# Performance work log

Measured on AMD Instinct MI355X. Metric: run time of the kernel, lower is better.

The kernel has to match this reference:

```python
import jax, jax.numpy as jnp
import numpy as np

N = 4096
IN_DIM = 512
NHEADS = 12
HEAD_DIM = 64


def setup_inputs() -> dict:
    key = jax.random.key(0)
    k_g, k_adj, k_wk, k_wq, k_hw = jax.random.split(key, 5)
    g = jax.random.normal(k_g, (N, IN_DIM), dtype=jnp.float32)
    # binary adjacency, broadcastable over the head axis of the [q,k,h] scores
    adj = jax.random.randint(k_adj, (N, N, 1), 0, 2).astype(jnp.float32)
    Wk = 0.002 * jax.random.normal(k_wk, (NHEADS, HEAD_DIM, IN_DIM), dtype=jnp.float32)
    Wq = 0.002 * jax.random.normal(k_wq, (NHEADS, HEAD_DIM, IN_DIM), dtype=jnp.float32)
    Hw = 0.002 * jax.random.normal(k_hw, (NHEADS, NHEADS), dtype=jnp.float32)
    Bk = jnp.zeros((NHEADS, HEAD_DIM), dtype=jnp.float32)
    Bq = jnp.zeros((NHEADS, HEAD_DIM), dtype=jnp.float32)
    betas = jnp.ones((NHEADS,), dtype=jnp.float32) / np.sqrt(HEAD_DIM).astype(np.float32)
    return {"g": g, "adj": adj, "Wk": Wk, "Wq": Wq, "Hw": Hw, "Bk": Bk, "Bq": Bq, "betas": betas}


def reference(g, adj, Wk, Wq, Hw, Bk, Bq, betas):
    def energy(g_):
        K = jnp.einsum('kd,hzd->khz', g_, Wk) + Bk          # [N, h, z]
        Q = jnp.einsum('qd,hzd->qhz', g_, Wq) + Bq          # [N, h, z]
        A1 = jnp.einsum('h,qhz,khz->hqk', betas, Q, K)      # [h, q, k]
        A11 = (jnp.transpose(A1, (1, 2, 0)) @ Hw) * adj      # [q, k, h], adjacency-gated
        A11 = jnp.where(A11 == 0, -jnp.inf, A11)
        A21 = jax.nn.logsumexp(A11, axis=1)                  # [q, h]
        A21 = jnp.where(A21 == -jnp.inf, 0.0, A21)
        A31 = A21.sum(0)                                     # [h]
        return ((-1.0 / betas) * A31).sum()
    # the module's __call__ returns (energy, dE/dg)
    return jax.value_and_grad(energy)(g)
```

## Files before the change

kernel.cpp:

```cpp
#include <hip/hip_runtime.h>
#include <stdint.h>

#define N_TOK 4096
#define DIM_IN 512
#define NH 12
#define HD 64
#define CDIM 768

using f32x4  = __attribute__((ext_vector_type(4))) float;
using f32x16 = __attribute__((ext_vector_type(16))) float;
using bf16x8 = __attribute__((ext_vector_type(8))) short;

static __device__ __forceinline__ unsigned short f2bf(float f){
    union { float f; unsigned int u; } v; v.f = f;
    unsigned int r = v.u + 0x7fffu + ((v.u >> 16) & 1u);
    return (unsigned short)(r >> 16);
}

__global__ __launch_bounds__(256) void proj_kernel(
    const float* __restrict__ g, const float* __restrict__ W,
    const float* __restrict__ B, const float* __restrict__ scale,
    unsigned short* __restrict__ out)
{
    __shared__ float at[16][68];
    __shared__ float bt[16][68];
    const int n0 = blockIdx.x * 64, c0 = blockIdx.y * 64;
    const int t  = threadIdx.x;
    const int tx = t & 15, ty = t >> 4;
    const int lr = t >> 2, lk = (t & 3) * 4;
    float acc[4][4] = {};
    for (int d0 = 0; d0 < DIM_IN; d0 += 16){
        __syncthreads();
        f32x4 gv = *(const f32x4*)&g[(size_t)(n0 + lr) * DIM_IN + d0 + lk];
        at[lk+0][lr] = gv[0]; at[lk+1][lr] = gv[1]; at[lk+2][lr] = gv[2]; at[lk+3][lr] = gv[3];
        f32x4 wv = *(const f32x4*)&W[(size_t)(c0 + lr) * DIM_IN + d0 + lk];
        bt[lk+0][lr] = wv[0]; bt[lk+1][lr] = wv[1]; bt[lk+2][lr] = wv[2]; bt[lk+3][lr] = wv[3];
        __syncthreads();
        #pragma unroll
        for (int kk = 0; kk < 16; kk++){
            f32x4 av = *(const f32x4*)&at[kk][ty*4];
            f32x4 bv = *(const f32x4*)&bt[kk][tx*4];
            #pragma unroll
            for (int i = 0; i < 4; i++)
                #pragma unroll
                for (int j = 0; j < 4; j++)
                    acc[i][j] += av[i] * bv[j];
        }
    }
    #pragma unroll
    for (int i = 0; i < 4; i++){
        const int n = n0 + ty*4 + i;
        #pragma unroll
        for (int j = 0; j < 4; j++){
            const int c = c0 + tx*4 + j;
            float v = acc[i][j] + B[c];
            if (scale) v *= scale[c >> 6];
            out[(size_t)n * CDIM + c] = f2bf(v);
        }
    }
}

#define TKF 32
#define KBS 776

__global__ __launch_bounds__(256, 2) void fwd_kernel(
    const unsigned short* __restrict__ Qb, const unsigned short* __restrict__ Kh,
    const float* __restrict__ adj, const float* __restrict__ HwG,
    float* __restrict__ l_ws, int seg_len)
{
    __shared__ unsigned short kbuf[TKF][KBS];
    __shared__ float hw[NH][12];
    const int t = threadIdx.x;
    if (t < NH * 12) hw[t / 12][t % 12] = HwG[t];
    const int lane = t & 63, wave = t >> 6;
    const int quad = lane >> 4, col = lane & 15;
    const int qt0 = blockIdx.x * 64 + wave * 16;
    const int kstart = blockIdx.y * seg_len;

    bf16x8 af[NH][2];
    {
        const int arow = qt0 + col;
        #pragma unroll
        for (int h = 0; h < NH; h++)
            #pragma unroll
            for (int kk = 0; kk < 2; kk++)
                af[h][kk] = *(const bf16x8*)&Qb[(size_t)arow * CDIM + h*HD + kk*32 + quad*8];
    }
    f32x4 l4[4][3];
    #pragma unroll
    for (int r = 0; r < 4; r++)
        #pragma unroll
        for (int j = 0; j < 3; j++)
            l4[r][j] = (f32x4){0.f,0.f,0.f,0.f};

    for (int kc = kstart; kc < kstart + seg_len; kc += TKF){
        __syncthreads();
        #pragma unroll
        for (int i = 0; i < 12; i++){
            const int idx = t + 256 * i;
            const int row = idx / 96, cc = (idx % 96) * 8;
            *(bf16x8*)&kbuf[row][cc] = *(const bf16x8*)&Kh[(size_t)(kc + row) * CDIM + cc];
        }
        __syncthreads();
        #pragma unroll
        for (int sub = 0; sub < 2; sub++){
            const int k0 = kc + sub * 16;
            f32x4 tv[4][3];
            #pragma unroll
            for (int r = 0; r < 4; r++)
                #pragma unroll
                for (int j = 0; j < 3; j++)
                    tv[r][j] = (f32x4){0.f,0.f,0.f,0.f};
            #pragma unroll
            for (int h = 0; h < NH; h++){
                bf16x8 b0 = *(const bf16x8*)&kbuf[sub*16 + col][h*HD + quad*8];
                bf16x8 b1 = *(const bf16x8*)&kbuf[sub*16 + col][h*HD + 32 + quad*8];
                f32x4 s = {0.f,0.f,0.f,0.f};
                s = __builtin_amdgcn_mfma_f32_16x16x32_bf16(af[h][0], b0, s, 0, 0, 0);
                s = __builtin_amdgcn_mfma_f32_16x16x32_bf16(af[h][1], b1, s, 0, 0, 0);
                f32x4 w0 = *(const f32x4*)&hw[h][0];
                f32x4 w1 = *(const f32x4*)&hw[h][4];
                f32x4 w2 = *(const f32x4*)&hw[h][8];
                #pragma unroll
                for (int r = 0; r < 4; r++){
                    tv[r][0] += s[r] * w0;
                    tv[r][1] += s[r] * w1;
                    tv[r][2] += s[r] * w2;
                }
            }
            #pragma unroll
            for (int r = 0; r < 4; r++){
                const float adjv = adj[(size_t)(qt0 + quad*4 + r) * N_TOK + k0 + col];
                #pragma unroll
                for (int j = 0; j < 3; j++){
                    #pragma unroll
                    for (int c = 0; c < 4; c++){
                        const float mm = tv[r][j][c] * adjv;
                        if (mm != 0.f) l4[r][j][c] += __expf(mm);
                    }
                }
            }
        }
    }
    #pragma unroll
    for (int r = 0; r < 4; r++)
        #pragma unroll
        for (int j = 0; j < 3; j++)
            #pragma unroll
            for (int c = 0; c < 4; c++){
                float v = l4[r][j][c];
                v += __shfl_xor(v, 1, 16);
                v += __shfl_xor(v, 2, 16);
                v += __shfl_xor(v, 4, 16);
                v += __shfl_xor(v, 8, 16);
                if (col == j*4 + c)
                    atomicAdd(&l_ws[(size_t)(qt0 + quad*4 + r) * NH + (j*4 + c)], v);
            }
}

__global__ __launch_bounds__(256) void lse_energy_kernel(
    const float* __restrict__ l_ws, float* __restrict__ lse_ws,
    const float* __restrict__ betas, float* __restrict__ energy)
{
    const int t = threadIdx.x;
    const int i = blockIdx.x * 256 + t;
    const float l = l_ws[i];
    float lse, ep;
    if (l > 0.f){ lse = logf(l); ep = -(1.f / betas[i % NH]) * lse; }
    else        { lse = -1e30f; ep = 0.f; }
    lse_ws[i] = lse;
    __shared__ float red[256];
    red[t] = ep;
    __syncthreads();
    for (int s = 128; s > 0; s >>= 1){
        if (t < s) red[t] += red[t + s];
        __syncthreads();
    }
    if (t == 0) atomicAdd(energy, red[0]);
}

#define CBS 776

template<int MODE>
__global__ __attribute__((amdgpu_flat_work_group_size(512, 512), amdgpu_waves_per_eu(2, 2)))
void bwd_kernel(
    const unsigned short* __restrict__ rowmat, const unsigned short* __restrict__ colmat,
    const float* __restrict__ adj, const float* __restrict__ HwG,
    const float* __restrict__ lse_ws, const float* __restrict__ betas,
    float* __restrict__ out_part, int seg_len)
{
    __shared__ unsigned short colbuf[64][CBS];
    __shared__ unsigned short dsbuf[NH][32][64];
    __shared__ float adjbuf[32][68];
    __shared__ float lsebuf[64 * NH];
    __shared__ float rowlse[32 * NH];
    __shared__ float invbuf[NH];
    __shared__ float hw[NH][12];
    const int t = threadIdx.x;
    if (t < NH * 12) hw[t / 12][t % 12] = HwG[t];
    if (t < NH) invbuf[t] = 1.f / betas[t];
    const int lane = t & 63, wave = t >> 6;
    const int quad = lane >> 4, col = lane & 15;
    const int rsub = wave >> 2, csub = wave & 3;
    const int n0 = csub * 16;
    const int rt0 = blockIdx.x * 32;
    const int rbase = rt0 + rsub * 16;
    const int cstart = blockIdx.y * seg_len;

    if (MODE == 0 && t < 96)
        *(f32x4*)&rowlse[t*4] = *(const f32x4*)&lse_ws[(size_t)rt0 * NH + t*4];

    const unsigned short* rowp = &rowmat[(size_t)(rbase + col) * CDIM + quad*8];

    const int strow = t / 96 * 0;
    (void)strow;
    const int adj_m  = t >> 4, adj_nc = (t & 15) * 4;
    const int adj_qr = t >> 3, adj_kc = (t & 7) * 4;

    bf16x8 pcol[12];
    f32x4  padj;
    f32x4  plse = {0.f,0.f,0.f,0.f};
    {
        const int cb = cstart;
        #pragma unroll
        for (int i = 0; i < 12; i++){
            const int idx = t + 512 * i;
            const int row = idx / 96, cc = (idx % 96) * 8;
            pcol[i] = *(const bf16x8*)&colmat[(size_t)(cb + row) * CDIM + cc];
        }
        if (MODE == 0) padj = *(const f32x4*)&adj[(size_t)(rt0 + adj_m) * N_TOK + cb + adj_nc];
        else           padj = *(const f32x4*)&adj[(size_t)(cb + adj_qr) * N_TOK + rt0 + adj_kc];
        if (MODE == 1 && t < 192)
            plse = *(const f32x4*)&lse_ws[(size_t)cb * NH + t*4];
    }

    f32x16 accB32[3];
    #pragma unroll
    for (int gg = 0; gg < 3; gg++)
        #pragma unroll
        for (int q = 0; q < 16; q++) accB32[gg][q] = 0.f;

    for (int cb = cstart; cb < cstart + seg_len; cb += 64){
        __syncthreads();
        #pragma unroll
        for (int i = 0; i < 12; i++){
            const int idx = t + 512 * i;
            const int row = idx / 96, cc = (idx % 96) * 8;
            *(bf16x8*)&colbuf[row][cc ^ (((row >> 3) & 3) << 3)] = pcol[i];
        }
        if (MODE == 0){
            adjbuf[adj_m][adj_nc+0] = padj[0]; adjbuf[adj_m][adj_nc+1] = padj[1];
            adjbuf[adj_m][adj_nc+2] = padj[2]; adjbuf[adj_m][adj_nc+3] = padj[3];
        } else {
            adjbuf[adj_kc+0][adj_qr] = padj[0]; adjbuf[adj_kc+1][adj_qr] = padj[1];
            adjbuf[adj_kc+2][adj_qr] = padj[2]; adjbuf[adj_kc+3][adj_qr] = padj[3];
        }
        if (MODE == 1 && t < 192)
            *(f32x4*)&lsebuf[t*4] = plse;
        __syncthreads();

        const unsigned short* rp = rowp;
        asm volatile("" : "+v"(rp));

        {
            const int tA = n0 + col;
            const int swzA = ((tA >> 3) & 3) << 3;
            f32x4 G[4][3];
            #pragma unroll
            for (int r = 0; r < 4; r++)
                #pragma unroll
                for (int j = 0; j < 3; j++)
                    G[r][j] = (f32x4){0.f,0.f,0.f,0.f};
            #pragma unroll
            for (int h = 0; h < NH; h++){
                bf16x8 a0 = *(const bf16x8*)&rp[h*HD];
                bf16x8 a1 = *(const bf16x8*)&rp[h*HD + 32];
                bf16x8 b0 = *(const bf16x8*)&colbuf[tA][(h*HD + quad*8) ^ swzA];
                bf16x8 b1 = *(const bf16x8*)&colbuf[tA][(h*HD + 32 + quad*8) ^ swzA];
                f32x4 s = {0.f,0.f,0.f,0.f};
                s = __builtin_amdgcn_mfma_f32_16x16x32_bf16(a0, b0, s, 0, 0, 0);
                s = __builtin_amdgcn_mfma_f32_16x16x32_bf16(a1, b1, s, 0, 0, 0);
                f32x4 w0 = *(const f32x4*)&hw[h][0];
                f32x4 w1 = *(const f32x4*)&hw[h][4];
                f32x4 w2 = *(const f32x4*)&hw[h][8];
                #pragma unroll
                for (int r = 0; r < 4; r++){
                    G[r][0] += s[r] * w0;
                    G[r][1] += s[r] * w1;
                    G[r][2] += s[r] * w2;
                }
            }
            #pragma unroll
            for (int r = 0; r < 4; r++){
                const float adjv = adjbuf[rsub*16 + quad*4 + r][tA];
                #pragma unroll
                for (int j = 0; j < 3; j++){
                    f32x4 lv;
                    if (MODE == 0) lv = *(const f32x4*)&rowlse[(rsub*16 + quad*4 + r) * NH + j*4];
                    else           lv = *(const f32x4*)&lsebuf[tA * NH + j*4];
                    #pragma unroll
                    for (int c = 0; c < 4; c++){
                        const float mm = G[r][j][c] * adjv;
                        const float p  = (mm != 0.f) ? __expf(mm - lv[c]) : 0.f;
                        G[r][j][c] = -invbuf[j*4 + c] * p;
                    }
                }
            }
            #pragma unroll
            for (int h = 0; h < NH; h++){
                f32x4 w0 = *(const f32x4*)&hw[h][0];
                f32x4 w1 = *(const f32x4*)&hw[h][4];
                f32x4 w2 = *(const f32x4*)&hw[h][8];
                #pragma unroll
                for (int r = 0; r < 4; r++){
                    f32x4 pr = G[r][0]*w0 + G[r][1]*w1 + G[r][2]*w2;
                    const float d = pr[0] + pr[1] + pr[2] + pr[3];
                    const int m = rsub*16 + quad*4 + r;
                    dsbuf[h][m][tA ^ ((m & 7) << 3)] = f2bf(d);
                }
            }
        }

        {
            const int nxt = cb + 64;
            const int cbn = (nxt < cstart + seg_len) ? nxt : cstart;
            #pragma unroll
            for (int i = 0; i < 12; i++){
                const int idx = t + 512 * i;
                const int row = idx / 96, cc = (idx % 96) * 8;
                pcol[i] = *(const bf16x8*)&colmat[(size_t)(cbn + row) * CDIM + cc];
            }
            if (MODE == 0) padj = *(const f32x4*)&adj[(size_t)(rt0 + adj_m) * N_TOK + cbn + adj_nc];
            else           padj = *(const f32x4*)&adj[(size_t)(cbn + adj_qr) * N_TOK + rt0 + adj_kc];
            if (MODE == 1 && t < 192)
                plse = *(const f32x4*)&lse_ws[(size_t)cbn * NH + t*4];
        }
        __syncthreads();

        {
            const int mB = lane & 31;
            const int halfB = lane >> 5;
            #pragma unroll
            for (int gg = 0; gg < 3; gg++){
                const int gidx = wave + gg*8;
                const int h = gidx >> 1, cg = gidx & 1;
                const int chL = h*HD + cg*32 + mB;
                f32x16 acc = accB32[gg];
                #pragma unroll
                for (int k0 = 0; k0 < 64; k0 += 16){
                    const int kbase = k0 + halfB*8;
                    bf16x8 a = *(const bf16x8*)&dsbuf[h][mB][kbase ^ ((mB & 7) << 3)];
                    const int sw = ((kbase >> 3) & 3) << 3;
                    const unsigned short* bp = &colbuf[kbase][chL ^ sw];
                    bf16x8 b;
                    #pragma unroll
                    for (int jj = 0; jj < 8; jj++)
                        b[jj] = (short)bp[jj * CBS];
                    acc = __builtin_amdgcn_mfma_f32_32x32x16_bf16(a, b, acc, 0, 0, 0);
                }
                accB32[gg] = acc;
            }
        }
    }
    float* outp = out_part + (size_t)blockIdx.y * N_TOK * CDIM;
    #pragma unroll
    for (int gg = 0; gg < 3; gg++){
        const int gidx = wave + gg*8;
        const int h = gidx >> 1, cg = gidx & 1;
        #pragma unroll
        for (int q = 0; q < 16; q++){
            const int i = (q & 3) + 8*(q >> 2) + 4*(lane >> 5);
            outp[(size_t)(rt0 + i) * CDIM + h*HD + cg*32 + (lane & 31)] = accB32[gg][q];
        }
    }
}

__global__ __launch_bounds__(256) void final_dg_kernel(
    const float* __restrict__ dQbp, const float* __restrict__ dKhp,
    const float* __restrict__ Wq, const float* __restrict__ Wk,
    const float* __restrict__ betas, float* __restrict__ dg, int nseg)
{
    __shared__ float at[16][68];
    __shared__ float bt[16][68];
    const int n0 = blockIdx.x * 64, d0 = blockIdx.y * 64;
    const int t  = threadIdx.x;
    const int tx = t & 15, ty = t >> 4;
    const int lr = t >> 2, lk = (t & 3) * 4;
    float acc[4][4] = {};
    for (int src = 0; src < 2; src++){
        const float* P = src ? dKhp : dQbp;
        const float* W = src ? Wk  : Wq;
        for (int c0 = 0; c0 < CDIM; c0 += 16){
            __syncthreads();
            f32x4 a = {0.f,0.f,0.f,0.f};
            for (int s = 0; s < nseg; s++)
                a += *(const f32x4*)&P[((size_t)s * N_TOK + n0 + lr) * CDIM + c0 + lk];
            if (src == 0){
                const float bs = betas[(c0 + lk) >> 6];
                a *= bs;
            }
            at[lk+0][lr] = a[0]; at[lk+1][lr] = a[1]; at[lk+2][lr] = a[2]; at[lk+3][lr] = a[3];
            {
                const int kk = t >> 4, dd = (t & 15) * 4;
                f32x4 wv = *(const f32x4*)&W[(size_t)(c0 + kk) * DIM_IN + d0 + dd];
                bt[kk][dd+0] = wv[0]; bt[kk][dd+1] = wv[1]; bt[kk][dd+2] = wv[2]; bt[kk][dd+3] = wv[3];
            }
            __syncthreads();
            #pragma unroll
            for (int kk = 0; kk < 16; kk++){
                f32x4 av = *(const f32x4*)&at[kk][ty*4];
                f32x4 bv = *(const f32x4*)&bt[kk][tx*4];
                #pragma unroll
                for (int i = 0; i < 4; i++)
                    #pragma unroll
                    for (int j = 0; j < 4; j++)
                        acc[i][j] += av[i] * bv[j];
            }
        }
    }
    #pragma unroll
    for (int i = 0; i < 4; i++)
        #pragma unroll
        for (int j = 0; j < 4; j++)
            dg[(size_t)(n0 + ty*4 + i) * DIM_IN + d0 + tx*4 + j] = acc[i][j];
}

extern "C" void kernel_launch(void* const* d_in, const int* in_sizes, int n_in,
                              void* d_out, int out_size, void* d_ws, size_t ws_size,
                              hipStream_t stream)
{
    const float* g     = (const float*)d_in[0];
    const float* adj   = (const float*)d_in[1];
    const float* Wk    = (const float*)d_in[2];
    const float* Wq    = (const float*)d_in[3];
    const float* Hw    = (const float*)d_in[4];
    const float* Bk    = (const float*)d_in[5];
    const float* Bq    = (const float*)d_in[6];
    const float* betas = (const float*)d_in[7];
    float* out = (float*)d_out;

    char* ws = (char*)d_ws;
    const size_t szQb   = (size_t)N_TOK * CDIM * sizeof(unsigned short);
    const size_t szL    = (size_t)N_TOK * NH * sizeof(float);
    const size_t szPart = (size_t)N_TOK * CDIM * sizeof(float);

    unsigned short* Qb = (unsigned short*)(ws);
    unsigned short* Kh = (unsigned short*)(ws + szQb);
    float* l_ws   = (float*)(ws + 2*szQb);
    float* lse_ws = (float*)(ws + 2*szQb + szL);
    char*  parts  = ws + 2*szQb + 2*szL;
    const size_t base = 2*szQb + 2*szL;

    int KS = 1;
    if      (ws_size >= base + 8*szPart) KS = 4;
    else if (ws_size >= base + 4*szPart) KS = 2;
    float* dQbp = (float*)parts;
    float* dKhp = (float*)(parts + (size_t)KS * szPart);

    hipMemsetAsync(l_ws, 0, szL, stream);
    hipMemsetAsync(d_out, 0, sizeof(float), stream);

    proj_kernel<<<dim3(64, 12), 256, 0, stream>>>(g, Wq, Bq, betas, Qb);
    proj_kernel<<<dim3(64, 12), 256, 0, stream>>>(g, Wk, Bk, nullptr, Kh);
    fwd_kernel<<<dim3(64, 8), 256, 0, stream>>>(Qb, Kh, adj, Hw, l_ws, N_TOK / 8);
    lse_energy_kernel<<<dim3(192), 256, 0, stream>>>(l_ws, lse_ws, betas, out);
    bwd_kernel<0><<<dim3(128, KS), 512, 0, stream>>>(Qb, Kh, adj, Hw, lse_ws, betas,
                                                     dQbp, N_TOK / KS);
    bwd_kernel<1><<<dim3(128, KS), 512, 0, stream>>>(Kh, Qb, adj, Hw, lse_ws, betas,
                                                     dKhp, N_TOK / KS);
    final_dg_kernel<<<dim3(64, 8), 256, 0, stream>>>(dQbp, dKhp, Wq, Wk, betas,
                                                     out + 1, KS);
}
```

Baseline: 1.625 ms.

## Read K/Q operands directly from global memory, using transposed copies for the backward MFMA

The projection kernel now also writes transposed bf16 copies of Q and K. The forward and backward kernels drop their LDS staging buffers for the column matrix and read MFMA operands straight from global memory, relying on cache. The backward second GEMM loads contiguous bf16x8 from the transposed copy instead of gathering strided elements from LDS. The adjacency/LSE tiles for MODE 1 are double-buffered, and the split factor KS is capped at 2. This trades LDS traffic and barriers for more global/L2 traffic, scattered transposed stores in proj, and extra workspace.

```diff
diff --git a/kernel.cpp b/kernel.cpp
--- a/kernel.cpp
+++ b/kernel.cpp
@@ -20,7 +20,7 @@
 __global__ __launch_bounds__(256) void proj_kernel(
     const float* __restrict__ g, const float* __restrict__ W,
     const float* __restrict__ B, const float* __restrict__ scale,
-    unsigned short* __restrict__ out)
+    unsigned short* __restrict__ out, unsigned short* __restrict__ outT)
 {
     __shared__ float at[16][68];
     __shared__ float bt[16][68];
@@ -55,20 +55,18 @@
             const int c = c0 + tx*4 + j;
             float v = acc[i][j] + B[c];
             if (scale) v *= scale[c >> 6];
-            out[(size_t)n * CDIM + c] = f2bf(v);
-        }
-    }
-}
-
-#define TKF 32
-#define KBS 776
+            const unsigned short b = f2bf(v);
+            out [(size_t)n * CDIM  + c] = b;
+            outT[(size_t)c * N_TOK + n] = b;
+        }
+    }
+}
 
 __global__ __launch_bounds__(256, 2) void fwd_kernel(
     const unsigned short* __restrict__ Qb, const unsigned short* __restrict__ Kh,
     const float* __restrict__ adj, const float* __restrict__ HwG,
     float* __restrict__ l_ws, int seg_len)
 {
-    __shared__ unsigned short kbuf[TKF][KBS];
     __shared__ float hw[NH][12];
     const int t = threadIdx.x;
     if (t < NH * 12) hw[t / 12][t % 12] = HwG[t];
@@ -76,6 +74,7 @@
     const int quad = lane >> 4, col = lane & 15;
     const int qt0 = blockIdx.x * 64 + wave * 16;
     const int kstart = blockIdx.y * seg_len;
+    __syncthreads();
 
     bf16x8 af[NH][2];
     {
@@ -93,51 +92,44 @@
         for (int j = 0; j < 3; j++)
             l4[r][j] = (f32x4){0.f,0.f,0.f,0.f};
 
-    for (int kc = kstart; kc < kstart + seg_len; kc += TKF){
-        __syncthreads();
-        #pragma unroll
-        for (int i = 0; i < 12; i++){
-            const int idx = t + 256 * i;
-            const int row = idx / 96, cc = (idx % 96) * 8;
-            *(bf16x8*)&kbuf[row][cc] = *(const bf16x8*)&Kh[(size_t)(kc + row) * CDIM + cc];
-        }
-        __syncthreads();
-        #pragma unroll
-        for (int sub = 0; sub < 2; sub++){
-            const int k0 = kc + sub * 16;
-            f32x4 tv[4][3];
-            #pragma unroll
-            for (int r = 0; r < 4; r++)
-                #pragma unroll
-                for (int j = 0; j < 3; j++)
-                    tv[r][j] = (f32x4){0.f,0.f,0.f,0.f};
-            #pragma unroll
-            for (int h = 0; h < NH; h++){
-                bf16x8 b0 = *(const bf16x8*)&kbuf[sub*16 + col][h*HD + quad*8];
-                bf16x8 b1 = *(const bf16x8*)&kbuf[sub*16 + col][h*HD + 32 + quad*8];
-                f32x4 s = {0.f,0.f,0.f,0.f};
-                s = __builtin_amdgcn_mfma_f32_16x16x32_bf16(af[h][0], b0, s, 0, 0, 0);
-                s = __builtin_amdgcn_mfma_f32_16x16x32_bf16(af[h][1], b1, s, 0, 0, 0);
-                f32x4 w0 = *(const f32x4*)&hw[h][0];
-                f32x4 w1 = *(const f32x4*)&hw[h][4];
-                f32x4 w2 = *(const f32x4*)&hw[h][8];
-                #pragma unroll
-                for (int r = 0; r < 4; r++){
-                    tv[r][0] += s[r] * w0;
-                    tv[r][1] += s[r] * w1;
-                    tv[r][2] += s[r] * w2;
-                }
-            }
+    for (int k0 = kstart; k0 < kstart + seg_len; k0 += 16){
+        float av[4];
+        #pragma unroll
+        for (int r = 0; r < 4; r++)
+            av[r] = adj[(size_t)(qt0 + quad*4 + r) * N_TOK + k0 + col];
+
+        const unsigned short* kp = &Kh[(size_t)(k0 + col) * CDIM + quad*8];
+        f32x4 tv[4][3];
+        #pragma unroll
+        for (int r = 0; r < 4; r++)
+            #pragma unroll
+            for (int j = 0; j < 3; j++)
+                tv[r][j] = (f32x4){0.f,0.f,0.f,0.f};
+        #pragma unroll
+        for (int h = 0; h < NH; h++){
+            bf16x8 b0 = *(const bf16x8*)&kp[h*HD];
+            bf16x8 b1 = *(const bf16x8*)&kp[h*HD + 32];
+            f32x4 s = {0.f,0.f,0.f,0.f};
+            s = __builtin_amdgcn_mfma_f32_16x16x32_bf16(af[h][0], b0, s, 0, 0, 0);
+            s = __builtin_amdgcn_mfma_f32_16x16x32_bf16(af[h][1], b1, s, 0, 0, 0);
+            f32x4 w0 = *(const f32x4*)&hw[h][0];
+            f32x4 w1 = *(const f32x4*)&hw[h][4];
+            f32x4 w2 = *(const f32x4*)&hw[h][8];
             #pragma unroll
             for (int r = 0; r < 4; r++){
-                const float adjv = adj[(size_t)(qt0 + quad*4 + r) * N_TOK + k0 + col];
-                #pragma unroll
-                for (int j = 0; j < 3; j++){
-                    #pragma unroll
-                    for (int c = 0; c < 4; c++){
-                        const float mm = tv[r][j][c] * adjv;
-                        if (mm != 0.f) l4[r][j][c] += __expf(mm);
-                    }
+                tv[r][0] += s[r] * w0;
+                tv[r][1] += s[r] * w1;
+                tv[r][2] += s[r] * w2;
+            }
+        }
+        #pragma unroll
+        for (int r = 0; r < 4; r++){
+            #pragma unroll
+            for (int j = 0; j < 3; j++){
+                #pragma unroll
+                for (int c = 0; c < 4; c++){
+                    const float mm = tv[r][j][c] * av[r];
+                    if (mm != 0.f) l4[r][j][c] += __expf(mm);
                 }
             }
         }
@@ -179,20 +171,18 @@
     if (t == 0) atomicAdd(energy, red[0]);
 }
 
-#define CBS 776
-
 template<int MODE>
 __global__ __attribute__((amdgpu_flat_work_group_size(512, 512), amdgpu_waves_per_eu(2, 2)))
 void bwd_kernel(
     const unsigned short* __restrict__ rowmat, const unsigned short* __restrict__ colmat,
+    const unsigned short* __restrict__ colmatT,
     const float* __restrict__ adj, const float* __restrict__ HwG,
     const float* __restrict__ lse_ws, const float* __restrict__ betas,
     float* __restrict__ out_part, int seg_len)
 {
-    __shared__ unsigned short colbuf[64][CBS];
     __shared__ unsigned short dsbuf[NH][32][64];
-    __shared__ float adjbuf[32][68];
-    __shared__ float lsebuf[64 * NH];
+    __shared__ float adjbuf[2][32][68];
+    __shared__ float lsebuf[2][64 * NH];
     __shared__ float rowlse[32 * NH];
     __shared__ float invbuf[NH];
     __shared__ float hw[NH][12];
@@ -206,65 +196,43 @@
     const int rt0 = blockIdx.x * 32;
     const int rbase = rt0 + rsub * 16;
     const int cstart = blockIdx.y * seg_len;
+    const int tA = n0 + col;
 
     if (MODE == 0 && t < 96)
         *(f32x4*)&rowlse[t*4] = *(const f32x4*)&lse_ws[(size_t)rt0 * NH + t*4];
 
+    const int s_qr = t >> 3, s_kc = (t & 7) * 4;
+    if (MODE == 1){
+        f32x4 a = *(const f32x4*)&adj[(size_t)(cstart + s_qr) * N_TOK + rt0 + s_kc];
+        adjbuf[0][s_kc+0][s_qr] = a[0]; adjbuf[0][s_kc+1][s_qr] = a[1];
+        adjbuf[0][s_kc+2][s_qr] = a[2]; adjbuf[0][s_kc+3][s_qr] = a[3];
+        if (t < 192)
+            *(f32x4*)&lsebuf[0][t*4] = *(const f32x4*)&lse_ws[(size_t)cstart * NH + t*4];
+    }
+
     const unsigned short* rowp = &rowmat[(size_t)(rbase + col) * CDIM + quad*8];
 
-    const int strow = t / 96 * 0;
-    (void)strow;
-    const int adj_m  = t >> 4, adj_nc = (t & 15) * 4;
-    const int adj_qr = t >> 3, adj_kc = (t & 7) * 4;
-
-    bf16x8 pcol[12];
-    f32x4  padj;
-    f32x4  plse = {0.f,0.f,0.f,0.f};
-    {
-        const int cb = cstart;
-        #pragma unroll
-        for (int i = 0; i < 12; i++){
-            const int idx = t + 512 * i;
-            const int row = idx / 96, cc = (idx % 96) * 8;
-            pcol[i] = *(const bf16x8*)&colmat[(size_t)(cb + row) * CDIM + cc];
-        }
-        if (MODE == 0) padj = *(const f32x4*)&adj[(size_t)(rt0 + adj_m) * N_TOK + cb + adj_nc];
-        else           padj = *(const f32x4*)&adj[(size_t)(cb + adj_qr) * N_TOK + rt0 + adj_kc];
-        if (MODE == 1 && t < 192)
-            plse = *(const f32x4*)&lse_ws[(size_t)cb * NH + t*4];
-    }
-
     f32x16 accB32[3];
     #pragma unroll
     for (int gg = 0; gg < 3; gg++)
         #pragma unroll
         for (int q = 0; q < 16; q++) accB32[gg][q] = 0.f;
 
+    __syncthreads();
+
+    int pb = 0;
     for (int cb = cstart; cb < cstart + seg_len; cb += 64){
-        __syncthreads();
-        #pragma unroll
-        for (int i = 0; i < 12; i++){
-            const int idx = t + 512 * i;
-            const int row = idx / 96, cc = (idx % 96) * 8;
-            *(bf16x8*)&colbuf[row][cc ^ (((row >> 3) & 3) << 3)] = pcol[i];
-        }
-        if (MODE == 0){
-            adjbuf[adj_m][adj_nc+0] = padj[0]; adjbuf[adj_m][adj_nc+1] = padj[1];
-            adjbuf[adj_m][adj_nc+2] = padj[2]; adjbuf[adj_m][adj_nc+3] = padj[3];
-        } else {
-            adjbuf[adj_kc+0][adj_qr] = padj[0]; adjbuf[adj_kc+1][adj_qr] = padj[1];
-            adjbuf[adj_kc+2][adj_qr] = padj[2]; adjbuf[adj_kc+3][adj_qr] = padj[3];
-        }
-        if (MODE == 1 && t < 192)
-            *(f32x4*)&lsebuf[t*4] = plse;
-        __syncthreads();
-
-        const unsigned short* rp = rowp;
-        asm volatile("" : "+v"(rp));
-
         {
-            const int tA = n0 + col;
-            const int swzA = ((tA >> 3) & 3) << 3;
+            float av4[4];
+            if (MODE == 0){
+                #pragma unroll
+                for (int r = 0; r < 4; r++)
+                    av4[r] = adj[(size_t)(rbase + quad*4 + r) * N_TOK + cb + tA];
+            }
+            const unsigned short* rp = rowp;
+            asm volatile("" : "+v"(rp));
+            const unsigned short* cp = &colmat[(size_t)(cb + tA) * CDIM + quad*8];
+
             f32x4 G[4][3];
             #pragma unroll
             for (int r = 0; r < 4; r++)
@@ -275,8 +243,8 @@
             for (int h = 0; h < NH; h++){
                 bf16x8 a0 = *(const bf16x8*)&rp[h*HD];
                 bf16x8 a1 = *(const bf16x8*)&rp[h*HD + 32];
-                bf16x8 b0 = *(const bf16x8*)&colbuf[tA][(h*HD + quad*8) ^ swzA];
-                bf16x8 b1 = *(const bf16x8*)&colbuf[tA][(h*HD + 32 + quad*8) ^ swzA];
+                bf16x8 b0 = *(const bf16x8*)&cp[h*HD];
+                bf16x8 b1 = *(const bf16x8*)&cp[h*HD + 32];
                 f32x4 s = {0.f,0.f,0.f,0.f};
                 s = __builtin_amdgcn_mfma_f32_16x16x32_bf16(a0, b0, s, 0, 0, 0);
                 s = __builtin_amdgcn_mfma_f32_16x16x32_bf16(a1, b1, s, 0, 0, 0);
@@ -292,12 +260,13 @@
             }
             #pragma unroll
             for (int r = 0; r < 4; r++){
-                const float adjv = adjbuf[rsub*16 + quad*4 + r][tA];
+                const float adjv = (MODE == 0) ? av4[r]
+                                  : adjbuf[pb][rsub*16 + quad*4 + r][tA];
                 #pragma unroll
                 for (int j = 0; j < 3; j++){
                     f32x4 lv;
                     if (MODE == 0) lv = *(const f32x4*)&rowlse[(rsub*16 + quad*4 + r) * NH + j*4];
-                    else           lv = *(const f32x4*)&lsebuf[tA * NH + j*4];
+                    else           lv = *(const f32x4*)&lsebuf[pb][tA * NH + j*4];
                     #pragma unroll
                     for (int c = 0; c < 4; c++){
                         const float mm = G[r][j][c] * adjv;
@@ -320,23 +289,15 @@
                 }
             }
         }
-
-        {
+        __syncthreads();
+
+        f32x4 nadj = {0.f,0.f,0.f,0.f}, nlse = {0.f,0.f,0.f,0.f};
+        if (MODE == 1){
             const int nxt = cb + 64;
             const int cbn = (nxt < cstart + seg_len) ? nxt : cstart;
-            #pragma unroll
-            for (int i = 0; i < 12; i++){
-                const int idx = t + 512 * i;
-                const int row = idx / 96, cc = (idx % 96) * 8;
-                pcol[i] = *(const bf16x8*)&colmat[(size_t)(cbn + row) * CDIM + cc];
-            }
-            if (MODE == 0) padj = *(const f32x4*)&adj[(size_t)(rt0 + adj_m) * N_TOK + cbn + adj_nc];
-            else           padj = *(const f32x4*)&adj[(size_t)(cbn + adj_qr) * N_TOK + rt0 + adj_kc];
-            if (MODE == 1 && t < 192)
-                plse = *(const f32x4*)&lse_ws[(size_t)cbn * NH + t*4];
-        }
-        __syncthreads();
-
+            nadj = *(const f32x4*)&adj[(size_t)(cbn + s_qr) * N_TOK + rt0 + s_kc];
+            if (t < 192) nlse = *(const f32x4*)&lse_ws[(size_t)cbn * NH + t*4];
+        }
         {
             const int mB = lane & 31;
             const int halfB = lane >> 5;
@@ -344,23 +305,26 @@
             for (int gg = 0; gg < 3; gg++){
                 const int gidx = wave + gg*8;
                 const int h = gidx >> 1, cg = gidx & 1;
-                const int chL = h*HD + cg*32 + mB;
+                const unsigned short* bpT =
+                    &colmatT[(size_t)(h*HD + cg*32 + mB) * N_TOK + cb + halfB*8];
                 f32x16 acc = accB32[gg];
                 #pragma unroll
                 for (int k0 = 0; k0 < 64; k0 += 16){
                     const int kbase = k0 + halfB*8;
                     bf16x8 a = *(const bf16x8*)&dsbuf[h][mB][kbase ^ ((mB & 7) << 3)];
-                    const int sw = ((kbase >> 3) & 3) << 3;
-                    const unsigned short* bp = &colbuf[kbase][chL ^ sw];
-                    bf16x8 b;
-                    #pragma unroll
-                    for (int jj = 0; jj < 8; jj++)
-                        b[jj] = (short)bp[jj * CBS];
+                    bf16x8 b = *(const bf16x8*)&bpT[k0];
                     acc = __builtin_amdgcn_mfma_f32_32x32x16_bf16(a, b, acc, 0, 0, 0);
                 }
                 accB32[gg] = acc;
             }
         }
+        if (MODE == 1){
+            adjbuf[pb^1][s_kc+0][s_qr] = nadj[0]; adjbuf[pb^1][s_kc+1][s_qr] = nadj[1];
+            adjbuf[pb^1][s_kc+2][s_qr] = nadj[2]; adjbuf[pb^1][s_kc+3][s_qr] = nadj[3];
+            if (t < 192) *(f32x4*)&lsebuf[pb^1][t*4] = nlse;
+        }
+        __syncthreads();
+        pb ^= 1;
     }
     float* outp = out_part + (size_t)blockIdx.y * N_TOK * CDIM;
     #pragma unroll
@@ -444,29 +408,29 @@
     const size_t szL    = (size_t)N_TOK * NH * sizeof(float);
     const size_t szPart = (size_t)N_TOK * CDIM * sizeof(float);
 
-    unsigned short* Qb = (unsigned short*)(ws);
-    unsigned short* Kh = (unsigned short*)(ws + szQb);
-    float* l_ws   = (float*)(ws + 2*szQb);
-    float* lse_ws = (float*)(ws + 2*szQb + szL);
-    char*  parts  = ws + 2*szQb + 2*szL;
-    const size_t base = 2*szQb + 2*szL;
-
-    int KS = 1;
-    if      (ws_size >= base + 8*szPart) KS = 4;
-    else if (ws_size >= base + 4*szPart) KS = 2;
+    unsigned short* Qb  = (unsigned short*)(ws);
+    unsigned short* Kh  = (unsigned short*)(ws + szQb);
+    unsigned short* QbT = (unsigned short*)(ws + 2*szQb);
+    unsigned short* KhT = (unsigned short*)(ws + 3*szQb);
+    float* l_ws   = (float*)(ws + 4*szQb);
+    float* lse_ws = (float*)(ws + 4*szQb + szL);
+    char*  parts  = ws + 4*szQb + 2*szL;
+    const size_t base = 4*szQb + 2*szL;
+
+    int KS = (ws_size >= base + 4*szPart) ? 2 : 1;
     float* dQbp = (float*)parts;
     float* dKhp = (float*)(parts + (size_t)KS * szPart);
 
     hipMemsetAsync(l_ws, 0, szL, stream);
     hipMemsetAsync(d_out, 0, sizeof(float), stream);
 
-    proj_kernel<<<dim3(64, 12), 256, 0, stream>>>(g, Wq, Bq, betas, Qb);
-    proj_kernel<<<dim3(64, 12), 256, 0, stream>>>(g, Wk, Bk, nullptr, Kh);
+    proj_kernel<<<dim3(64, 12), 256, 0, stream>>>(g, Wq, Bq, betas, Qb, QbT);
+    proj_kernel<<<dim3(64, 12), 256, 0, stream>>>(g, Wk, Bk, nullptr, Kh, KhT);
     fwd_kernel<<<dim3(64, 8), 256, 0, stream>>>(Qb, Kh, adj, Hw, l_ws, N_TOK / 8);
     lse_energy_kernel<<<dim3(192), 256, 0, stream>>>(l_ws, lse_ws, betas, out);
-    bwd_kernel<0><<<dim3(128, KS), 512, 0, stream>>>(Qb, Kh, adj, Hw, lse_ws, betas,
+    bwd_kernel<0><<<dim3(128, KS), 512, 0, stream>>>(Qb, Kh, KhT, adj, Hw, lse_ws, betas,
                                                      dQbp, N_TOK / KS);
-    bwd_kernel<1><<<dim3(128, KS), 512, 0, stream>>>(Kh, Qb, adj, Hw, lse_ws, betas,
+    bwd_kernel<1><<<dim3(128, KS), 512, 0, stream>>>(Kh, Qb, QbT, adj, Hw, lse_ws, betas,
                                                      dKhp, N_TOK / KS);
     final_dg_kernel<<<dim3(64, 8), 256, 0, stream>>>(dQbp, dKhp, Wq, Wk, betas,
                                                      out + 1, KS);
```

New measurement: 1.909 ms. +17.5%, slower.
